# Optimization experiments

Hardware: AMD Instinct MI355X
Metric: run time of the kernel (lower is better)

The kernel has to match this reference:

```python
import jax, jax.numpy as jnp
import numpy as np

K = 512
H = 8

def setup_inputs() -> dict:
    key = jax.random.key(0)
    ks = jax.random.split(key, 6)
    b, t, k = 4, 2048, K
    scale = 1.0 / np.sqrt(k)
    return {
        "x": jax.random.normal(ks[0], (b, t, k), dtype=jnp.float32),
        "Wq": jax.random.normal(ks[1], (k, k), dtype=jnp.float32) * scale,
        "Wk": jax.random.normal(ks[2], (k, k), dtype=jnp.float32) * scale,
        "Wv": jax.random.normal(ks[3], (k, k), dtype=jnp.float32) * scale,
        "Wo": jax.random.normal(ks[4], (k, k), dtype=jnp.float32) * scale,
        "bo": jax.random.normal(ks[5], (k,), dtype=jnp.float32) * 0.01,
    }

def reference(x, Wq, Wk, Wv, Wo, bo):
    b, t, k = x.shape
    h = H
    s = k // h
    # nn.Linear: y = x @ W.T ; weights stored [out, in]
    q = (x @ Wq.T).reshape(b, t, h, s)
    kk = (x @ Wk.T).reshape(b, t, h, s)
    v = (x @ Wv.T).reshape(b, t, h, s)
    # scores: note original divides by sqrt(k) (full model dim), not sqrt(s)
    dot = jnp.einsum("bqhs,bkhs->bhqk", q, kk) / jnp.sqrt(jnp.float32(k))
    attn = jax.nn.softmax(dot, axis=-1)
    out = jnp.einsum("bhqk,bkhs->bqhs", attn, v).reshape(b, t, k)
    return out @ Wo.T + bo
```

## Files before the change

### kernel.cpp

```cpp
#include <hip/hip_runtime.h>

typedef _Float16 f16;
typedef _Float16 f16x8 __attribute__((ext_vector_type(8)));
typedef _Float16 f16x4 __attribute__((ext_vector_type(4)));
typedef float    f32x4 __attribute__((ext_vector_type(4)));
typedef __fp16   fp16x2 __attribute__((ext_vector_type(2)));

#define MFMA(a,b,c) __builtin_amdgcn_mfma_f32_16x16x32_f16((a),(b),(c),0,0,0)

#if __has_builtin(__builtin_amdgcn_exp2f)
#define EXP2(x) __builtin_amdgcn_exp2f(x)
#else
#define EXP2(x) exp2f(x)
#endif

__device__ __forceinline__ void gl_lds16(const void* g, void* l) {
  __builtin_amdgcn_global_load_lds(
      (__attribute__((address_space(1))) void*)(void*)(g),
      (__attribute__((address_space(3))) void*)(l),
      16, 0, 0);
}

__device__ __forceinline__ int SWZ(int row) {
  return ((row & 3) | ((row >> 1) & 4)) << 4;
}

__global__ __launch_bounds__(256) void k_convert(
    const float* __restrict__ x, const float* __restrict__ Wq,
    const float* __restrict__ Wk, const float* __restrict__ Wv,
    const float* __restrict__ Wo,
    f16* __restrict__ x_h, f16* __restrict__ wqkv_h, f16* __restrict__ wo_h) {
  const int XQ    = (8192 * 512) / 4;
  const int WQKVQ = (1536 * 512) / 4;
  const int WOQ   = (512 * 512) / 4;
  const int total = XQ + WQKVQ + WOQ;
  for (int q = blockIdx.x * blockDim.x + threadIdx.x; q < total;
       q += gridDim.x * blockDim.x) {
    const float* src;
    f16* dst;
    if (q < XQ) {
      src = x + q * 4;
      dst = x_h + q * 4;
    } else if (q < XQ + WQKVQ) {
      int j  = q - XQ;
      int r  = j >> 7;
      int c0 = (j & 127) * 4;
      const float* w = (r < 512) ? Wq : (r < 1024) ? Wk : Wv;
      src = w + (r & 511) * 512 + c0;
      dst = wqkv_h + j * 4;
    } else {
      int j = q - XQ - WQKVQ;
      src = Wo + j * 4;
      dst = wo_h + j * 4;
    }
    float4 v = *(const float4*)src;
    f16x4 o = {(f16)v.x, (f16)v.y, (f16)v.z, (f16)v.w};
    *(f16x4*)dst = o;
  }
}

__device__ __forceinline__ void gemm_core(const f16* __restrict__ A,
                                          const f16* __restrict__ B,
                                          int bm, int bn, f32x4 (&acc)[4][4]) {
  __shared__ f16 As[2][128 * 64];
  __shared__ f16 Bs[2][128 * 64];
  const int tid  = threadIdx.x;
  const int lane = tid & 63;
  const int w    = tid >> 6;
  const int wr   = (w >> 1) & 1, wc = w & 1;
  const int r0   = tid >> 3;
  const int cb   = (tid & 7) << 4;

  auto stage = [&](int buf, int kt) {
#pragma unroll
    for (int inst = 0; inst < 4; ++inst) {
      const int row  = inst * 32 + r0;
      const int csrc = cb ^ ((row & 7) << 4);
      gl_lds16(A + (bm + row) * 512 + kt + (csrc >> 1),
               (char*)As[buf] + inst * 4096 + w * 1024);
      gl_lds16(B + (bn + row) * 512 + kt + (csrc >> 1),
               (char*)Bs[buf] + inst * 4096 + w * 1024);
    }
  };

  stage(0, 0);
#pragma unroll
  for (int t = 0; t < 8; ++t) {
    const int cur = t & 1;
    asm volatile("s_waitcnt vmcnt(0)" ::: "memory");
    __builtin_amdgcn_s_barrier();
    __builtin_amdgcn_sched_barrier(0);
    if (t < 7) stage(cur ^ 1, (t + 1) * 64);
    f16x8 af[4][2], bf[4][2];
#pragma unroll
    for (int i = 0; i < 4; ++i) {
      const int ra = wr * 64 + i * 16 + (lane & 15);
      const int rb = wc * 64 + i * 16 + (lane & 15);
#pragma unroll
      for (int ks = 0; ks < 2; ++ks) {
        const int cc = ks * 64 + ((lane >> 4) << 4);
        af[i][ks] = *(const f16x8*)((const char*)As[cur] + ra * 128 + (cc ^ ((ra & 7) << 4)));
        bf[i][ks] = *(const f16x8*)((const char*)Bs[cur] + rb * 128 + (cc ^ ((rb & 7) << 4)));
      }
    }
    __builtin_amdgcn_s_setprio(1);
#pragma unroll
    for (int i = 0; i < 4; ++i)
#pragma unroll
      for (int j = 0; j < 4; ++j) {
        acc[i][j] = MFMA(af[i][0], bf[j][0], acc[i][j]);
        acc[i][j] = MFMA(af[i][1], bf[j][1], acc[i][j]);
      }
    __builtin_amdgcn_s_setprio(0);
  }
}

__global__ __launch_bounds__(256) void k_gemm_qkv(
    const f16* __restrict__ A, const f16* __restrict__ B,
    f16* __restrict__ q_h, f16* __restrict__ k_h, f16* __restrict__ vt_h) {
  const int bm = blockIdx.x * 128;
  const int bn = blockIdx.y * 128;
  f32x4 acc[4][4] = {};
  gemm_core(A, B, bm, bn, acc);

  const int tid  = threadIdx.x;
  const int lane = tid & 63;
  const int w    = tid >> 6;
  const int wr   = (w >> 1) & 1, wc = w & 1;
  const float qscale = 0.044194173824159216f * 1.4426950408889634f;
#pragma unroll
  for (int i = 0; i < 4; ++i) {
    const int m0 = bm + wr * 64 + i * 16 + ((lane >> 4) << 2);
#pragma unroll
    for (int j = 0; j < 4; ++j) {
      const int n   = bn + wc * 64 + j * 16 + (lane & 15);
      const int sec = n >> 9;
      const int nn  = n & 511;
      const int h   = nn >> 6, s = nn & 63;
#pragma unroll
      for (int r = 0; r < 4; ++r) {
        const int m = m0 + r;
        const int b = m >> 11, t = m & 2047;
        const int bh = b * 8 + h;
        const float v = acc[i][j][r];
        if (sec == 0)
          q_h[(bh * 2048 + t) * 64 + s] = (f16)(v * qscale);
        else if (sec == 1)
          k_h[(bh * 2048 + t) * 64 + s] = (f16)v;
        else
          vt_h[(bh * 64 + s) * 2048 + t] = (f16)v;
      }
    }
  }
}

__global__ __launch_bounds__(512, 2) void k_attn(
    const f16* __restrict__ q_h, const f16* __restrict__ k_h,
    const f16* __restrict__ vt_h, f16* __restrict__ a_h) {
  __shared__ char smem[65536];

  const int tid  = threadIdx.x;
  const int lane = tid & 63;
  const int w    = tid >> 6;
  const int g    = w >> 2;
  const int wg   = w & 3;

  int id = blockIdx.x;
  id = (id & 7) * 64 + (id >> 3);
  const int qt = (id & 15) * 128;
  const int bh = id >> 4;

  const f16* qb = q_h + (size_t)bh * 2048 * 64;
  const f16* kb = k_h + (size_t)bh * 2048 * 64;
  const f16* vb = vt_h + (size_t)bh * 64 * 2048;

  auto KsP = [&](int grp, int buf) { return smem + (grp * 2 + buf) * 8192; };
  auto VsP = [&](int grp, int buf) { return smem + 32768 + (grp * 2 + buf) * 8192; };

  f16x8 qf[2][2];
#pragma unroll
  for (int i = 0; i < 2; ++i) {
    const int qrow = qt + wg * 32 + i * 16 + (lane & 15);
#pragma unroll
    for (int ks = 0; ks < 2; ++ks)
      qf[i][ks] = *(const f16x8*)(qb + qrow * 64 + ks * 32 + ((lane >> 4) << 3));
  }

  f32x4 oacc[2][4] = {};
  f32x4 lrun[2]    = {};

  const int gt  = tid & 255;
  const int r0  = gt >> 3;
  const int cbb = (tid & 7) << 4;

  const f16 one = (f16)1.0f;
  const f16x8 ones = {one, one, one, one, one, one, one, one};

  auto stage = [&](int buf, int t) {
    const int ktv = g * 1024 + t * 64;
#pragma unroll
    for (int inst = 0; inst < 2; ++inst) {
      const int row  = inst * 32 + r0;
      const int csrc = cbb ^ SWZ(row);
      gl_lds16(kb + (ktv + row) * 64 + (csrc >> 1),
               KsP(g, buf) + inst * 4096 + wg * 1024);
      gl_lds16(vb + row * 2048 + ktv + (csrc >> 1),
               VsP(g, buf) + inst * 4096 + wg * 1024);
    }
  };

  auto pack4 = [](float a, float b, float c, float d) -> unsigned long long {
    union { fp16x2 h2[2]; unsigned long long u; } t;
    t.h2[0] = __builtin_amdgcn_cvt_pkrtz(a, b);
    t.h2[1] = __builtin_amdgcn_cvt_pkrtz(c, d);
    return t.u;
  };

  auto tile = [&](const char* ksb, const char* vsb) {
    f16x8 kf[4][2];
    const int m  = lane & 15;
    const int hi = lane >> 4;
#pragma unroll
    for (int n = 0; n < 4; ++n) {
      const int row = ((n >> 1) << 5) + ((m >> 2) << 3) + ((n & 1) << 2) + (m & 3);
      const int sw  = SWZ(row);
#pragma unroll
      for (int ks = 0; ks < 2; ++ks) {
        const int c = (ks * 64 + (hi << 4)) ^ sw;
        kf[n][ks] = *(const f16x8*)(ksb + row * 128 + c);
      }
    }
    f32x4 sf[2][4];
    __builtin_amdgcn_s_setprio(1);
#pragma unroll
    for (int i = 0; i < 2; ++i)
#pragma unroll
      for (int n = 0; n < 4; ++n) {
        f32x4 s = {0.f, 0.f, 0.f, 0.f};
        s = MFMA(kf[n][0], qf[i][0], s);
        s = MFMA(kf[n][1], qf[i][1], s);
        sf[i][n] = s;
      }
    __builtin_amdgcn_s_setprio(0);
    f16x8 pa[2][2];
#pragma unroll
    for (int i = 0; i < 2; ++i)
#pragma unroll
      for (int ks = 0; ks < 2; ++ks) {
        union { unsigned long long u[2]; f16x8 v; } u;
        u.u[0] = pack4(EXP2(sf[i][2 * ks][0]), EXP2(sf[i][2 * ks][1]),
                       EXP2(sf[i][2 * ks][2]), EXP2(sf[i][2 * ks][3]));
        u.u[1] = pack4(EXP2(sf[i][2 * ks + 1][0]), EXP2(sf[i][2 * ks + 1][1]),
                       EXP2(sf[i][2 * ks + 1][2]), EXP2(sf[i][2 * ks + 1][3]));
        pa[i][ks] = u.v;
      }
    __builtin_amdgcn_s_setprio(1);
#pragma unroll
    for (int i = 0; i < 2; ++i) {
      lrun[i] = MFMA(pa[i][0], ones, lrun[i]);
      lrun[i] = MFMA(pa[i][1], ones, lrun[i]);
    }
#pragma unroll
    for (int n = 0; n < 4; ++n) {
      const int row = n * 16 + m;
      const int sw  = SWZ(row);
      const f16x8 vf0 = *(const f16x8*)(vsb + row * 128 + ((hi << 4) ^ sw));
      const f16x8 vf1 = *(const f16x8*)(vsb + row * 128 + ((64 + (hi << 4)) ^ sw));
#pragma unroll
      for (int i = 0; i < 2; ++i) {
        oacc[i][n] = MFMA(pa[i][0], vf0, oacc[i][n]);
        oacc[i][n] = MFMA(pa[i][1], vf1, oacc[i][n]);
      }
    }
    __builtin_amdgcn_s_setprio(0);
  };

  stage(0, 0);
  for (int j = 0; j < 16; ++j) {
    const int cur = j & 1;
    asm volatile("s_waitcnt vmcnt(0)" ::: "memory");
    __builtin_amdgcn_s_barrier();
    __builtin_amdgcn_sched_barrier(0);
    if (j < 15) stage(cur ^ 1, j + 1);
    tile(KsP(g, cur), VsP(g, cur));
  }

  __syncthreads();
  float* Ol = (float*)smem;
  float* ll = (float*)(smem + 34816);

  if (g == 1) {
#pragma unroll
    for (int i = 0; i < 2; ++i)
#pragma unroll
      for (int r = 0; r < 4; ++r) {
        const int q = wg * 32 + i * 16 + ((lane >> 4) << 2) + r;
#pragma unroll
        for (int n = 0; n < 4; ++n)
          Ol[q * 68 + n * 16 + (lane & 15)] = oacc[i][n][r];
        if ((lane & 15) == 0) ll[q] = lrun[i][r];
      }
  }
  __syncthreads();
  if (g == 0) {
    const int b2 = bh >> 3, h2 = bh & 7;
#pragma unroll
    for (int i = 0; i < 2; ++i)
#pragma unroll
      for (int r = 0; r < 4; ++r) {
        const int q  = wg * 32 + i * 16 + ((lane >> 4) << 2) + r;
        const float rl = 1.0f / (lrun[i][r] + ll[q]);
        const int qrow = qt + q;
#pragma unroll
        for (int n = 0; n < 4; ++n) {
          const int s = n * 16 + (lane & 15);
          const float o = oacc[i][n][r] + Ol[q * 68 + s];
          a_h[(size_t)(b2 * 2048 + qrow) * 512 + h2 * 64 + s] = (f16)(o * rl);
        }
      }
  }
}

__global__ __launch_bounds__(256) void k_gemm_out(
    const f16* __restrict__ A, const f16* __restrict__ B,
    const float* __restrict__ bo, float* __restrict__ out) {
  const int bm = blockIdx.x * 128;
  const int bn = blockIdx.y * 128;
  f32x4 acc[4][4] = {};
  gemm_core(A, B, bm, bn, acc);

  const int tid  = threadIdx.x;
  const int lane = tid & 63;
  const int w    = tid >> 6;
  const int wr   = (w >> 1) & 1, wc = w & 1;
#pragma unroll
  for (int i = 0; i < 4; ++i) {
    const int m0 = bm + wr * 64 + i * 16 + ((lane >> 4) << 2);
#pragma unroll
    for (int j = 0; j < 4; ++j) {
      const int n = bn + wc * 64 + j * 16 + (lane & 15);
      const float bias = bo[n];
#pragma unroll
      for (int r = 0; r < 4; ++r)
        out[(size_t)(m0 + r) * 512 + n] = acc[i][j][r] + bias;
    }
  }
}

extern "C" void kernel_launch(void* const* d_in, const int* in_sizes, int n_in,
                              void* d_out, int out_size, void* d_ws, size_t ws_size,
                              hipStream_t stream) {
  const float* x  = (const float*)d_in[0];
  const float* Wq = (const float*)d_in[1];
  const float* Wk = (const float*)d_in[2];
  const float* Wv = (const float*)d_in[3];
  const float* Wo = (const float*)d_in[4];
  const float* bo = (const float*)d_in[5];
  float* out = (float*)d_out;

  char* ws = (char*)d_ws;
  f16* x_h    = (f16*)(ws);
  f16* wqkv_h = (f16*)(ws + 8388608);
  f16* wo_h   = (f16*)(ws + 9961472);
  f16* q_h    = (f16*)(ws + 10485760);
  f16* k_h    = (f16*)(ws + 18874368);
  f16* vt_h   = (f16*)(ws + 27262976);
  f16* a_h    = (f16*)(ws + 35651584);
  (void)ws_size; (void)in_sizes; (void)n_in; (void)out_size;

  k_convert<<<2048, 256, 0, stream>>>(x, Wq, Wk, Wv, Wo, x_h, wqkv_h, wo_h);
  k_gemm_qkv<<<dim3(64, 12), 256, 0, stream>>>(x_h, wqkv_h, q_h, k_h, vt_h);
  k_attn<<<512, 512, 0, stream>>>(q_h, k_h, vt_h, a_h);
  k_gemm_out<<<dim3(64, 4), 256, 0, stream>>>(a_h, wo_h, bo, out);
}
```

Before: 85.90 us.

## Double attention query tile per block to 256 rows, halving grid size

Each attention block now handles 256 query rows instead of 128, with each wave holding 64 query rows (4 MFMA row tiles) against the same staged K/V tiles. This halves K/V global loads and LDS staging per unit of work and raises MFMA work per LDS fragment read. The cross-group reduction epilogue is split into two passes so it fits the shared memory. The cost is higher register pressure (doubled accumulators and score fragments) and only 256 blocks, which may underfill the 256 CUs or hurt occupancy.

After: 85.84 us. About the same (-0.1%).

```diff
diff --git a/kernel.cpp b/kernel.cpp
--- a/kernel.cpp
+++ b/kernel.cpp
@@ -166,28 +166,31 @@
   const int wg   = w & 3;
 
   int id = blockIdx.x;
-  id = (id & 7) * 64 + (id >> 3);
-  const int qt = (id & 15) * 128;
-  const int bh = id >> 4;
+  id = (id & 7) * 32 + (id >> 3);
+  const int qt = (id & 7) * 256;
+  const int bh = id >> 3;
 
   const f16* qb = q_h + (size_t)bh * 2048 * 64;
   const f16* kb = k_h + (size_t)bh * 2048 * 64;
   const f16* vb = vt_h + (size_t)bh * 64 * 2048;
 
-  auto KsP = [&](int grp, int buf) { return smem + (grp * 2 + buf) * 8192; };
-  auto VsP = [&](int grp, int buf) { return smem + 32768 + (grp * 2 + buf) * 8192; };
-
-  f16x8 qf[2][2];
-#pragma unroll
-  for (int i = 0; i < 2; ++i) {
-    const int qrow = qt + wg * 32 + i * 16 + (lane & 15);
+  auto KsP = [&](int grp, int buf) { return smem + grp * 32768 + buf * 16384; };
+  auto VsP = [&](int grp, int buf) { return smem + grp * 32768 + buf * 16384 + 8192; };
+
+  const int m  = lane & 15;
+  const int hi = lane >> 4;
+
+  f16x8 qf[4][2];
+#pragma unroll
+  for (int i = 0; i < 4; ++i) {
+    const int qrow = qt + wg * 64 + i * 16 + m;
 #pragma unroll
     for (int ks = 0; ks < 2; ++ks)
-      qf[i][ks] = *(const f16x8*)(qb + qrow * 64 + ks * 32 + ((lane >> 4) << 3));
-  }
-
-  f32x4 oacc[2][4] = {};
-  f32x4 lrun[2]    = {};
+      qf[i][ks] = *(const f16x8*)(qb + qrow * 64 + ks * 32 + hi * 8);
+  }
+
+  f32x4 oacc[4][4] = {};
+  f32x4 lrun[4]    = {};
 
   const int gt  = tid & 255;
   const int r0  = gt >> 3;
@@ -218,8 +221,6 @@
 
   auto tile = [&](const char* ksb, const char* vsb) {
     f16x8 kf[4][2];
-    const int m  = lane & 15;
-    const int hi = lane >> 4;
 #pragma unroll
     for (int n = 0; n < 4; ++n) {
       const int row = ((n >> 1) << 5) + ((m >> 2) << 3) + ((n & 1) << 2) + (m & 3);
@@ -230,10 +231,10 @@
         kf[n][ks] = *(const f16x8*)(ksb + row * 128 + c);
       }
     }
-    f32x4 sf[2][4];
+    f32x4 sf[4][4];
     __builtin_amdgcn_s_setprio(1);
 #pragma unroll
-    for (int i = 0; i < 2; ++i)
+    for (int i = 0; i < 4; ++i)
 #pragma unroll
       for (int n = 0; n < 4; ++n) {
         f32x4 s = {0.f, 0.f, 0.f, 0.f};
@@ -242,9 +243,9 @@
         sf[i][n] = s;
       }
     __builtin_amdgcn_s_setprio(0);
-    f16x8 pa[2][2];
-#pragma unroll
-    for (int i = 0; i < 2; ++i)
+    f16x8 pa[4][2];
+#pragma unroll
+    for (int i = 0; i < 4; ++i)
 #pragma unroll
       for (int ks = 0; ks < 2; ++ks) {
         union { unsigned long long u[2]; f16x8 v; } u;
@@ -256,7 +257,7 @@
       }
     __builtin_amdgcn_s_setprio(1);
 #pragma unroll
-    for (int i = 0; i < 2; ++i) {
+    for (int i = 0; i < 4; ++i) {
       lrun[i] = MFMA(pa[i][0], ones, lrun[i]);
       lrun[i] = MFMA(pa[i][1], ones, lrun[i]);
     }
@@ -267,7 +268,7 @@
       const f16x8 vf0 = *(const f16x8*)(vsb + row * 128 + ((hi << 4) ^ sw));
       const f16x8 vf1 = *(const f16x8*)(vsb + row * 128 + ((64 + (hi << 4)) ^ sw));
 #pragma unroll
-      for (int i = 0; i < 2; ++i) {
+      for (int i = 0; i < 4; ++i) {
         oacc[i][n] = MFMA(pa[i][0], vf0, oacc[i][n]);
         oacc[i][n] = MFMA(pa[i][1], vf1, oacc[i][n]);
       }
@@ -287,37 +288,42 @@
 
   __syncthreads();
   float* Ol = (float*)smem;
-  float* ll = (float*)(smem + 34816);
-
-  if (g == 1) {
-#pragma unroll
-    for (int i = 0; i < 2; ++i)
-#pragma unroll
-      for (int r = 0; r < 4; ++r) {
-        const int q = wg * 32 + i * 16 + ((lane >> 4) << 2) + r;
-#pragma unroll
-        for (int n = 0; n < 4; ++n)
-          Ol[q * 68 + n * 16 + (lane & 15)] = oacc[i][n][r];
-        if ((lane & 15) == 0) ll[q] = lrun[i][r];
-      }
-  }
-  __syncthreads();
-  if (g == 0) {
-    const int b2 = bh >> 3, h2 = bh & 7;
-#pragma unroll
-    for (int i = 0; i < 2; ++i)
-#pragma unroll
-      for (int r = 0; r < 4; ++r) {
-        const int q  = wg * 32 + i * 16 + ((lane >> 4) << 2) + r;
-        const float rl = 1.0f / (lrun[i][r] + ll[q]);
-        const int qrow = qt + q;
-#pragma unroll
-        for (int n = 0; n < 4; ++n) {
-          const int s = n * 16 + (lane & 15);
-          const float o = oacc[i][n][r] + Ol[q * 68 + s];
-          a_h[(size_t)(b2 * 2048 + qrow) * 512 + h2 * 64 + s] = (f16)(o * rl);
+  float* l1 = (float*)(smem + 34816);
+
+  const int b2 = bh >> 3, h2 = bh & 7;
+#pragma unroll
+  for (int p = 0; p < 2; ++p) {
+    if (g == 1 && (wg >> 1) == p) {
+#pragma unroll
+      for (int i = 0; i < 4; ++i)
+#pragma unroll
+        for (int r = 0; r < 4; ++r) {
+          const int ql = (wg * 64 + i * 16 + hi * 4 + r) & 127;
+#pragma unroll
+          for (int n = 0; n < 4; ++n)
+            Ol[ql * 68 + n * 16 + m] = oacc[i][n][r];
+          if (m == 0) l1[ql] = lrun[i][r];
         }
-      }
+    }
+    __syncthreads();
+    if (g == 0 && (wg >> 1) == p) {
+#pragma unroll
+      for (int i = 0; i < 4; ++i)
+#pragma unroll
+        for (int r = 0; r < 4; ++r) {
+          const int qg = wg * 64 + i * 16 + hi * 4 + r;
+          const int ql = qg & 127;
+          const float rl = 1.0f / (lrun[i][r] + l1[ql]);
+          const int qrow = qt + qg;
+#pragma unroll
+          for (int n = 0; n < 4; ++n) {
+            const int s = n * 16 + m;
+            const float o = oacc[i][n][r] + Ol[ql * 68 + s];
+            a_h[(size_t)(b2 * 2048 + qrow) * 512 + h2 * 64 + s] = (f16)(o * rl);
+          }
+        }
+    }
+    __syncthreads();
   }
 }
 
@@ -370,6 +376,6 @@
 
   k_convert<<<2048, 256, 0, stream>>>(x, Wq, Wk, Wv, Wo, x_h, wqkv_h, wo_h);
   k_gemm_qkv<<<dim3(64, 12), 256, 0, stream>>>(x_h, wqkv_h, q_h, k_h, vt_h);
-  k_attn<<<512, 512, 0, stream>>>(q_h, k_h, vt_h, a_h);
+  k_attn<<<256, 512, 0, stream>>>(q_h, k_h, vt_h, a_h);
   k_gemm_out<<<dim3(64, 4), 256, 0, stream>>>(a_h, wo_h, bo, out);
 }
```
